# Performance work log

Hardware: AMD Instinct MI355X
Metric: run time of the kernel (lower is better)

The kernel has to match this reference:

```python
import jax, jax.numpy as jnp
import numpy as np

NODE_DIM = 8
IN_EDGE_DIM = 4
OUT_EDGE_DIM = 4
HID = 16
N_NODES = 100000
N_EDGES = 3200000
LN_EPS = 1e-5


def _layer_norm(h, gamma, beta):
    mu = jnp.mean(h, axis=-1, keepdims=True)
    var = jnp.mean(jnp.square(h - mu), axis=-1, keepdims=True)
    return (h - mu) * jax.lax.rsqrt(var + LN_EPS) * gamma + beta


def setup_inputs() -> dict:
    key = jax.random.key(0)
    ks = jax.random.split(key, 12)
    in_dim = NODE_DIM * 2 + IN_EDGE_DIM  # 20
    x = jax.random.normal(ks[0], (N_NODES, NODE_DIM), dtype=jnp.float32)
    edge_index = jax.random.randint(ks[1], (2, N_EDGES), 0, N_NODES, dtype=jnp.int64)
    edge_attr = jax.random.normal(ks[2], (N_EDGES, IN_EDGE_DIM), dtype=jnp.float32)
    # MLP params (Kaiming-uniform-ish scaling like torch defaults)
    def lin(k, fan_in, fan_out):
        lim = 1.0 / np.sqrt(fan_in)
        kw, kb = jax.random.split(k)
        W = jax.random.uniform(kw, (fan_in, fan_out), minval=-lim, maxval=lim, dtype=jnp.float32)
        b = jax.random.uniform(kb, (fan_out,), minval=-lim, maxval=lim, dtype=jnp.float32)
        return W, b
    W1, b1 = lin(ks[3], in_dim, HID)
    W2, b2 = lin(ks[4], HID, HID)
    W3, b3 = lin(ks[5], HID, OUT_EDGE_DIM)
    g1 = jnp.ones((HID,), jnp.float32); be1 = jnp.zeros((HID,), jnp.float32)
    g2 = jnp.ones((HID,), jnp.float32); be2 = jnp.zeros((HID,), jnp.float32)
    return {"x": x, "edge_index": edge_index, "edge_attr": edge_attr,
            "W1": W1, "b1": b1, "g1": g1, "be1": be1,
            "W2": W2, "b2": b2, "g2": g2, "be2": be2,
            "W3": W3, "b3": b3}


def reference(x, edge_index, edge_attr, W1, b1, g1, be1, W2, b2, g2, be2, W3, b3):
    frm = edge_index[0]
    to = edge_index[1]
    # gather node features for both endpoints, concat with edge features: [E, 2*node_dim+in_edge_dim]
    inpt = jnp.concatenate([x[frm], x[to], edge_attr.astype(jnp.float32)], axis=1)
    h = _layer_norm(jax.nn.relu(inpt @ W1 + b1), g1, be1)
    h = _layer_norm(jax.nn.relu(h @ W2 + b2), g2, be2)
    return h @ W3 + b3  # [E, out_edge_dim]
```

## Files before the change

### kernel.cpp

```cpp
#include <hip/hip_runtime.h>
#include <stdint.h>


using u16 = unsigned short;
using u32 = uint32_t;
typedef __attribute__((ext_vector_type(4))) float f32x4;
typedef __attribute__((ext_vector_type(8))) short bf16x8;
typedef __attribute__((ext_vector_type(2))) __bf16 bf16x2;

__device__ __forceinline__ float bf2f(u16 u) { return __uint_as_float(((u32)u) << 16); }
__device__ __forceinline__ float bflo(u32 u) { return __uint_as_float(u << 16); }
__device__ __forceinline__ float bfhi(u32 u) { return __uint_as_float(u & 0xFFFF0000u); }
__device__ __forceinline__ u32 f2bf(float f) {
    u32 u = __float_as_uint(f);
    return (u + 0x7FFFu + ((u >> 16) & 1u)) >> 16;
}
__device__ __forceinline__ u32 pkbf(float a, float b) {
    bf16x2 t;
    t.x = (__bf16)a;
    t.y = (__bf16)b;
    return __builtin_bit_cast(u32, t);
}
__device__ __forceinline__ float ldw(const void* p, int i, bool bf) {
    return bf ? bf2f(((const u16*)p)[i]) : ((const float*)p)[i];
}

#define WB_W1 0
#define WB_B1 320
#define WB_W2 336
#define WB_B2 592
#define WB_W3 608
#define WB_B3 672
#define WB_TOT 704
#define FQ_A1H 0
#define FQ_A1L 512
#define FQ_A2H 1024
#define FQ_A2L 1536
#define FQ_A3H 2048
#define FQ_A3L 2560
#define FB_OFF (WB_TOT + 1536)

__global__ __launch_bounds__(256)
void probe_convert(const int* __restrict__ ei, int n_pairs,
                   const void* W1, const void* b1, const void* g1, const void* be1,
                   const void* W2, const void* b2, const void* g2, const void* be2,
                   const void* W3, const void* b3,
                   int* __restrict__ flags, float* __restrict__ wb) {
    bool bf = (((const u32*)g1)[0] == 0x3F803F80u);
    __shared__ int s;
    if (threadIdx.x == 0) s = 0;
    __syncthreads();
    int limit = n_pairs < 2048 ? n_pairs : 2048;
    int found = 0;
    for (int i = threadIdx.x; i < limit; i += blockDim.x)
        if (ei[2 * i + 1] != 0) found = 1;
    if (found) s = 1;
    __syncthreads();
    if (threadIdx.x == 0) { flags[0] = s; flags[1] = bf ? 1 : 0; }

    int t = threadIdx.x;
    for (int i = t; i < 320; i += 256) wb[WB_W1 + i] = ldw(W1, i, bf);
    if (t < 16) wb[WB_B1 + t] = ldw(b1, t, bf);
    {
        int k = t >> 4;
        wb[WB_W2 + t] = ldw(g1, k, bf) * ldw(W2, t, bf);
    }
    if (t < 16) {
        float acc = ldw(b2, t, bf);
        for (int k = 0; k < 16; k++) acc = fmaf(ldw(be1, k, bf), ldw(W2, k * 16 + t, bf), acc);
        wb[WB_B2 + t] = acc;
    }
    if (t < 64) {
        int k = t >> 2;
        wb[WB_W3 + t] = ldw(g2, k, bf) * ldw(W3, t, bf);
    }
    if (t < 4) {
        float acc = ldw(b3, t, bf);
        for (int k = 0; k < 16; k++) acc = fmaf(ldw(be2, k, bf), ldw(W3, k * 4 + t, bf), acc);
        wb[WB_B3 + t] = acc;
    }
    if (t >= 4 && t < 32) wb[672 + t] = 0.f;

    __syncthreads();

    u16* fq = (u16*)(wb + WB_TOT);
    for (int i = t; i < 512; i += 256) {
        int l = i >> 3, j = i & 7;
        int m = l & 15, g = l >> 4;
        int k = g * 8 + j;
        int kk = k & 15;
        float w1 = (k < 20) ? wb[WB_W1 + k * 16 + m] : 0.f;
        u16 h1 = (u16)f2bf(w1);
        fq[FQ_A1H + i] = h1;
        fq[FQ_A1L + i] = (u16)f2bf(w1 - bf2f(h1));
        float w2 = wb[WB_W2 + kk * 16 + m];
        u16 h2 = (u16)f2bf(w2);
        fq[FQ_A2H + i] = h2;
        fq[FQ_A2L + i] = (u16)f2bf(w2 - bf2f(h2));
        float w3 = (m < 4) ? wb[WB_W3 + kk * 4 + m] : 0.f;
        u16 h3 = (u16)f2bf(w3);
        fq[FQ_A3H + i] = h3;
        fq[FQ_A3L + i] = (u16)f2bf(w3 - bf2f(h3));
    }
    {
        float* fbv = wb + FB_OFF;
        int l = t >> 2, r = t & 3;
        int row = ((l >> 4) << 2) + r;
        fbv[t] = wb[WB_B1 + row];
        fbv[256 + t] = wb[WB_B2 + row];
        fbv[512 + t] = (row < 4) ? wb[WB_B3 + row] : 0.f;
    }
}

__device__ __forceinline__ void ln16(f32x4 d, float& h0, float& h1, float& h2, float& h3) {
    f32x4 z = {0.f, 0.f, 0.f, 0.f};
    d = __builtin_elementwise_max(d, z);
    float s = (d.x + d.y) + (d.z + d.w);
    float q = fmaf(d.x, d.x, fmaf(d.y, d.y, fmaf(d.z, d.z, d.w * d.w)));
    s += __shfl_xor(s, 16);
    q += __shfl_xor(q, 16);
    s += __shfl_xor(s, 32);
    q += __shfl_xor(q, 32);
    float mu = s * 0.0625f;
    float var = fmaf(-mu, mu, q * 0.0625f);
    float r = rsqrtf(var + 1e-5f);
    float nb = -mu * r;
    h0 = fmaf(d.x, r, nb);
    h1 = fmaf(d.y, r, nb);
    h2 = fmaf(d.z, r, nb);
    h3 = fmaf(d.w, r, nb);
}

__device__ __forceinline__ bf16x8 redist_split(float h0, float h1, float h2, float h3,
                                               int n, int g) {
    u32 hi01 = pkbf(h0, h1), hi23 = pkbf(h2, h3);
    float r0 = h0 - bflo(hi01);
    float r1 = h1 - bfhi(hi01);
    float r2 = h2 - bflo(hi23);
    float r3 = h3 - bfhi(hi23);
    u32 lo01 = pkbf(r0, r1), lo23 = pkbf(r2, r3);
    int srcA = n + (((g & 1) << 1) << 4);
    int srcB = srcA + 16;
    u32 hA01 = (u32)__shfl((int)hi01, srcA);
    u32 hA23 = (u32)__shfl((int)hi23, srcA);
    u32 lA01 = (u32)__shfl((int)lo01, srcA);
    u32 lA23 = (u32)__shfl((int)lo23, srcA);
    u32 hB01 = (u32)__shfl((int)hi01, srcB);
    u32 hB23 = (u32)__shfl((int)hi23, srcB);
    u32 lB01 = (u32)__shfl((int)lo01, srcB);
    u32 lB23 = (u32)__shfl((int)lo23, srcB);
    bool hi = (g < 2);
    uint4 uu = make_uint4(hi ? hA01 : lA01, hi ? hA23 : lA23,
                          hi ? hB01 : lB01, hi ? hB23 : lB23);
    return __builtin_bit_cast(bf16x8, uu);
}

#define TPW 8

__global__ __launch_bounds__(256, 4)
void edge_mlp_mfma(const void* __restrict__ x, const int* __restrict__ ei,
                   const void* __restrict__ ea, const float* __restrict__ wb,
                   const int* __restrict__ flags, void* __restrict__ out, int n_edges) {
    const bool idx32 = flags[0] != 0;
    const bool bf = flags[1] != 0;

    const int lane = threadIdx.x & 63;
    const int n = lane & 15;
    const int g = lane >> 4;

    const u16* fq = (const u16*)(wb + WB_TOT);
    bf16x8 A1h = ((const bf16x8*)fq)[0 * 64 + lane];
    bf16x8 A1l = ((const bf16x8*)fq)[1 * 64 + lane];
    bf16x8 A2h = ((const bf16x8*)fq)[2 * 64 + lane];
    bf16x8 A2l = ((const bf16x8*)fq)[3 * 64 + lane];
    bf16x8 A3h = ((const bf16x8*)fq)[4 * 64 + lane];
    bf16x8 A3l = ((const bf16x8*)fq)[5 * 64 + lane];
    const f32x4* fb = (const f32x4*)(wb + FB_OFF);
    f32x4 pb1 = fb[lane];
    f32x4 pb2 = fb[64 + lane];
    f32x4 pb3 = fb[128 + lane];

    const int ntiles = (n_edges + 15) >> 4;
    const int wflat = blockIdx.x * 4 + (threadIdx.x >> 6);
    const int t0 = wflat * TPW;

#pragma unroll 1
    for (int ti = 0; ti < TPW; ++ti) {
        int tile = t0 + ti;
        if (tile >= ntiles) break;

        int e = (tile << 4) + n;
        bool ev = e < n_edges;

        int idx = 0;
        if (g < 2 && ev) {
            size_t col = (g == 0) ? (size_t)e : ((size_t)n_edges + (size_t)e);
            idx = idx32 ? ei[col] : ei[2 * col];
        }

        f32x4 d1 = pb1;
        if (bf) {
            uint4 raw = make_uint4(0u, 0u, 0u, 0u);
            if (g < 2) {
                raw = ((const uint4*)x)[idx];
            } else if (g == 2 && ev) {
                uint2 r = ((const uint2*)ea)[e];
                raw.x = r.x;
                raw.y = r.y;
            }
            d1 = __builtin_amdgcn_mfma_f32_16x16x32_bf16(
                A1h, __builtin_bit_cast(bf16x8, raw), d1, 0, 0, 0);
        } else {
            float f0 = 0.f, f1 = 0.f, f2 = 0.f, f3 = 0.f;
            float f4 = 0.f, f5 = 0.f, f6 = 0.f, f7 = 0.f;
            if (g < 2) {
                const float4* xp = (const float4*)x;
                float4 a = xp[2 * idx], b = xp[2 * idx + 1];
                f0 = a.x; f1 = a.y; f2 = a.z; f3 = a.w;
                f4 = b.x; f5 = b.y; f6 = b.z; f7 = b.w;
            } else if (g == 2 && ev) {
                float4 r = ((const float4*)ea)[e];
                f0 = r.x; f1 = r.y; f2 = r.z; f3 = r.w;
            }
            u32 h01 = pkbf(f0, f1), h23 = pkbf(f2, f3);
            u32 h45 = pkbf(f4, f5), h67 = pkbf(f6, f7);
            u32 l01 = pkbf(f0 - bflo(h01), f1 - bfhi(h01));
            u32 l23 = pkbf(f2 - bflo(h23), f3 - bfhi(h23));
            u32 l45 = pkbf(f4 - bflo(h45), f5 - bfhi(h45));
            u32 l67 = pkbf(f6 - bflo(h67), f7 - bfhi(h67));
            bf16x8 Bh = __builtin_bit_cast(bf16x8, make_uint4(h01, h23, h45, h67));
            bf16x8 Bl = __builtin_bit_cast(bf16x8, make_uint4(l01, l23, l45, l67));
            d1 = __builtin_amdgcn_mfma_f32_16x16x32_bf16(A1h, Bh, d1, 0, 0, 0);
            d1 = __builtin_amdgcn_mfma_f32_16x16x32_bf16(A1h, Bl, d1, 0, 0, 0);
            d1 = __builtin_amdgcn_mfma_f32_16x16x32_bf16(A1l, Bh, d1, 0, 0, 0);
        }

        float h0, h1, h2, h3;
        ln16(d1, h0, h1, h2, h3);

        bf16x8 f2v = redist_split(h0, h1, h2, h3, n, g);
        f32x4 d2 = pb2;
        d2 = __builtin_amdgcn_mfma_f32_16x16x32_bf16(A2h, f2v, d2, 0, 0, 0);
        d2 = __builtin_amdgcn_mfma_f32_16x16x32_bf16(A2l, f2v, d2, 0, 0, 0);
        float z0, z1, z2, z3;
        ln16(d2, z0, z1, z2, z3);

        bf16x8 f3v = redist_split(z0, z1, z2, z3, n, g);
        f32x4 d3 = pb3;
        d3 = __builtin_amdgcn_mfma_f32_16x16x32_bf16(A3h, f3v, d3, 0, 0, 0);
        d3 = __builtin_amdgcn_mfma_f32_16x16x32_bf16(A3l, f3v, d3, 0, 0, 0);

        if (g == 0 && ev) {
            if (bf) {
                u32 p0 = pkbf(d3.x, d3.y);
                u32 p1 = pkbf(d3.z, d3.w);
                ((uint2*)out)[e] = make_uint2(p0, p1);
            } else {
                ((float4*)out)[e] = make_float4(d3.x, d3.y, d3.z, d3.w);
            }
        }
    }
}

extern "C" void kernel_launch(void* const* d_in, const int* in_sizes, int n_in,
                              void* d_out, int out_size, void* d_ws, size_t ws_size,
                              hipStream_t stream) {
    const void* x  = d_in[0];
    const int* ei  = (const int*)d_in[1];
    const void* ea = d_in[2];

    int n_edges = in_sizes[1] / 2;

    int* flags = (int*)d_ws;
    float* wb = (float*)((char*)d_ws + 64);

    probe_convert<<<1, 256, 0, stream>>>(ei, n_edges,
                                         d_in[3], d_in[4], d_in[5], d_in[6],
                                         d_in[7], d_in[8], d_in[9], d_in[10],
                                         d_in[11], d_in[12], flags, wb);

    int ntiles = (n_edges + 15) / 16;
    int mblocks = (ntiles + 4 * TPW - 1) / (4 * TPW);
    edge_mlp_mfma<<<mblocks, 256, 0, stream>>>(x, ei, ea, wb, flags, d_out, n_edges);
}
```

Baseline: 214.4 us.

## Repack layer-2/3 weights to drop cross-lane shuffles and use branchless gathers

Reorders the layer-2 and layer-3 bf16 hi/lo weight fragments so each lane's own LayerNorm outputs (hi and lo parts) can feed the next MFMA directly as the B operand. This removes the eight ds_bpermute-style shuffles per layer that redistributed activations across lanes. The input gather becomes branchless: lanes that have no real data read from a zeroed scratch region in the weight buffer, and out-of-range edge indices are clamped. The tile loop is also unrolled by 2, which adds code size and register pressure and relies on the zero region staying zero.

```diff
diff --git a/kernel.cpp b/kernel.cpp
--- a/kernel.cpp
+++ b/kernel.cpp
@@ -32,12 +32,13 @@
 #define WB_W3 608
 #define WB_B3 672
 #define WB_TOT 704
+#define WB_ZRG 676
 #define FQ_A1H 0
 #define FQ_A1L 512
-#define FQ_A2H 1024
-#define FQ_A2L 1536
-#define FQ_A3H 2048
-#define FQ_A3L 2560
+#define FQ_A2X 1024
+#define FQ_A2Y 1536
+#define FQ_A3X 2048
+#define FQ_A3Y 2560
 #define FB_OFF (WB_TOT + 1536)
 
 __global__ __launch_bounds__(256)
@@ -87,20 +88,25 @@
     for (int i = t; i < 512; i += 256) {
         int l = i >> 3, j = i & 7;
         int m = l & 15, g = l >> 4;
-        int k = g * 8 + j;
-        int kk = k & 15;
-        float w1 = (k < 20) ? wb[WB_W1 + k * 16 + m] : 0.f;
+        int k1 = g * 8 + j;
+        float w1 = (k1 < 20) ? wb[WB_W1 + k1 * 16 + m] : 0.f;
         u16 h1 = (u16)f2bf(w1);
         fq[FQ_A1H + i] = h1;
         fq[FQ_A1L + i] = (u16)f2bf(w1 - bf2f(h1));
-        float w2 = wb[WB_W2 + kk * 16 + m];
+
+        int k2 = g * 4 + (j & 3);
+        int part = j >> 2;
+        float w2 = wb[WB_W2 + k2 * 16 + m];
         u16 h2 = (u16)f2bf(w2);
-        fq[FQ_A2H + i] = h2;
-        fq[FQ_A2L + i] = (u16)f2bf(w2 - bf2f(h2));
-        float w3 = (m < 4) ? wb[WB_W3 + kk * 4 + m] : 0.f;
+        u16 l2v = (u16)f2bf(w2 - bf2f(h2));
+        fq[FQ_A2X + i] = part ? l2v : h2;
+        fq[FQ_A2Y + i] = part ? h2 : l2v;
+
+        float w3 = (m < 4) ? wb[WB_W3 + k2 * 4 + m] : 0.f;
         u16 h3 = (u16)f2bf(w3);
-        fq[FQ_A3H + i] = h3;
-        fq[FQ_A3L + i] = (u16)f2bf(w3 - bf2f(h3));
+        u16 l3v = (u16)f2bf(w3 - bf2f(h3));
+        fq[FQ_A3X + i] = part ? l3v : h3;
+        fq[FQ_A3Y + i] = part ? h3 : l3v;
     }
     {
         float* fbv = wb + FB_OFF;
@@ -131,28 +137,11 @@
     h3 = fmaf(d.w, r, nb);
 }
 
-__device__ __forceinline__ bf16x8 redist_split(float h0, float h1, float h2, float h3,
-                                               int n, int g) {
+__device__ __forceinline__ bf16x8 packB(float h0, float h1, float h2, float h3) {
     u32 hi01 = pkbf(h0, h1), hi23 = pkbf(h2, h3);
-    float r0 = h0 - bflo(hi01);
-    float r1 = h1 - bfhi(hi01);
-    float r2 = h2 - bflo(hi23);
-    float r3 = h3 - bfhi(hi23);
-    u32 lo01 = pkbf(r0, r1), lo23 = pkbf(r2, r3);
-    int srcA = n + (((g & 1) << 1) << 4);
-    int srcB = srcA + 16;
-    u32 hA01 = (u32)__shfl((int)hi01, srcA);
-    u32 hA23 = (u32)__shfl((int)hi23, srcA);
-    u32 lA01 = (u32)__shfl((int)lo01, srcA);
-    u32 lA23 = (u32)__shfl((int)lo23, srcA);
-    u32 hB01 = (u32)__shfl((int)hi01, srcB);
-    u32 hB23 = (u32)__shfl((int)hi23, srcB);
-    u32 lB01 = (u32)__shfl((int)lo01, srcB);
-    u32 lB23 = (u32)__shfl((int)lo23, srcB);
-    bool hi = (g < 2);
-    uint4 uu = make_uint4(hi ? hA01 : lA01, hi ? hA23 : lA23,
-                          hi ? hB01 : lB01, hi ? hB23 : lB23);
-    return __builtin_bit_cast(bf16x8, uu);
+    u32 lo01 = pkbf(h0 - bflo(hi01), h1 - bfhi(hi01));
+    u32 lo23 = pkbf(h2 - bflo(hi23), h3 - bfhi(hi23));
+    return __builtin_bit_cast(bf16x8, make_uint4(hi01, hi23, lo01, lo23));
 }
 
 #define TPW 8
@@ -171,63 +160,64 @@
     const u16* fq = (const u16*)(wb + WB_TOT);
     bf16x8 A1h = ((const bf16x8*)fq)[0 * 64 + lane];
     bf16x8 A1l = ((const bf16x8*)fq)[1 * 64 + lane];
-    bf16x8 A2h = ((const bf16x8*)fq)[2 * 64 + lane];
-    bf16x8 A2l = ((const bf16x8*)fq)[3 * 64 + lane];
-    bf16x8 A3h = ((const bf16x8*)fq)[4 * 64 + lane];
-    bf16x8 A3l = ((const bf16x8*)fq)[5 * 64 + lane];
+    bf16x8 A2x = ((const bf16x8*)fq)[2 * 64 + lane];
+    bf16x8 A2y = ((const bf16x8*)fq)[3 * 64 + lane];
+    bf16x8 A3x = ((const bf16x8*)fq)[4 * 64 + lane];
+    bf16x8 A3y = ((const bf16x8*)fq)[5 * 64 + lane];
     const f32x4* fb = (const f32x4*)(wb + FB_OFF);
     f32x4 pb1 = fb[lane];
     f32x4 pb2 = fb[64 + lane];
     f32x4 pb3 = fb[128 + lane];
 
+    const char* zrg = (const char*)(wb + WB_ZRG);
+    const size_t eoff = (g == 1) ? (size_t)n_edges : 0;
+
     const int ntiles = (n_edges + 15) >> 4;
     const int wflat = blockIdx.x * 4 + (threadIdx.x >> 6);
     const int t0 = wflat * TPW;
 
-#pragma unroll 1
+#pragma unroll 2
     for (int ti = 0; ti < TPW; ++ti) {
         int tile = t0 + ti;
         if (tile >= ntiles) break;
 
         int e = (tile << 4) + n;
         bool ev = e < n_edges;
+        int ec = ev ? e : (n_edges - 1);
 
         int idx = 0;
-        if (g < 2 && ev) {
-            size_t col = (g == 0) ? (size_t)e : ((size_t)n_edges + (size_t)e);
+        if (g < 2) {
+            size_t col = eoff + (size_t)ec;
             idx = idx32 ? ei[col] : ei[2 * col];
         }
 
         f32x4 d1 = pb1;
         if (bf) {
-            uint4 raw = make_uint4(0u, 0u, 0u, 0u);
-            if (g < 2) {
-                raw = ((const uint4*)x)[idx];
-            } else if (g == 2 && ev) {
-                uint2 r = ((const uint2*)ea)[e];
-                raw.x = r.x;
-                raw.y = r.y;
-            }
+            const uint4* pA = (g < 2)
+                ? (const uint4*)((const char*)x + (size_t)idx * 16)
+                : (const uint4*)zrg;
+            const uint2* pE = (g == 2)
+                ? (const uint2*)((const char*)ea + (size_t)ec * 8)
+                : (const uint2*)zrg;
+            uint4 r16 = *pA;
+            uint2 r8 = *pE;
+            uint4 braw = make_uint4(r16.x | r8.x, r16.y | r8.y, r16.z, r16.w);
             d1 = __builtin_amdgcn_mfma_f32_16x16x32_bf16(
-                A1h, __builtin_bit_cast(bf16x8, raw), d1, 0, 0, 0);
+                A1h, __builtin_bit_cast(bf16x8, braw), d1, 0, 0, 0);
         } else {
-            float f0 = 0.f, f1 = 0.f, f2 = 0.f, f3 = 0.f;
-            float f4 = 0.f, f5 = 0.f, f6 = 0.f, f7 = 0.f;
-            if (g < 2) {
-                const float4* xp = (const float4*)x;
-                float4 a = xp[2 * idx], b = xp[2 * idx + 1];
-                f0 = a.x; f1 = a.y; f2 = a.z; f3 = a.w;
-                f4 = b.x; f5 = b.y; f6 = b.z; f7 = b.w;
-            } else if (g == 2 && ev) {
-                float4 r = ((const float4*)ea)[e];
-                f0 = r.x; f1 = r.y; f2 = r.z; f3 = r.w;
-            }
-            u32 h01 = pkbf(f0, f1), h23 = pkbf(f2, f3);
-            u32 h45 = pkbf(f4, f5), h67 = pkbf(f6, f7);
-            u32 l01 = pkbf(f0 - bflo(h01), f1 - bfhi(h01));
-            u32 l23 = pkbf(f2 - bflo(h23), f3 - bfhi(h23));
-            u32 l45 = pkbf(f4 - bflo(h45), f5 - bfhi(h45));
-            u32 l67 = pkbf(f6 - bflo(h67), f7 - bfhi(h67));
+            const float4* pA = (g < 2)
+                ? (const float4*)((const char*)x + (size_t)idx * 32)
+                : ((g == 2) ? (const float4*)((const char*)ea + (size_t)ec * 16)
+                            : (const float4*)zrg);
+            const float4* pB = (g < 2) ? (pA + 1) : (const float4*)zrg;
+            float4 a = *pA;
+            float4 b = *pB;
+            u32 h01 = pkbf(a.x, a.y), h23 = pkbf(a.z, a.w);
+            u32 h45 = pkbf(b.x, b.y), h67 = pkbf(b.z, b.w);
+            u32 l01 = pkbf(a.x - bflo(h01), a.y - bfhi(h01));
+            u32 l23 = pkbf(a.z - bflo(h23), a.w - bfhi(h23));
+            u32 l45 = pkbf(b.x - bflo(h45), b.y - bfhi(h45));
+            u32 l67 = pkbf(b.z - bflo(h67), b.w - bfhi(h67));
             bf16x8 Bh = __builtin_bit_cast(bf16x8, make_uint4(h01, h23, h45, h67));
             bf16x8 Bl = __builtin_bit_cast(bf16x8, make_uint4(l01, l23, l45, l67));
             d1 = __builtin_amdgcn_mfma_f32_16x16x32_bf16(A1h, Bh, d1, 0, 0, 0);
@@ -238,17 +228,17 @@
         float h0, h1, h2, h3;
         ln16(d1, h0, h1, h2, h3);
 
-        bf16x8 f2v = redist_split(h0, h1, h2, h3, n, g);
+        bf16x8 B2 = packB(h0, h1, h2, h3);
         f32x4 d2 = pb2;
-        d2 = __builtin_amdgcn_mfma_f32_16x16x32_bf16(A2h, f2v, d2, 0, 0, 0);
-        d2 = __builtin_amdgcn_mfma_f32_16x16x32_bf16(A2l, f2v, d2, 0, 0, 0);
+        d2 = __builtin_amdgcn_mfma_f32_16x16x32_bf16(A2x, B2, d2, 0, 0, 0);
+        d2 = __builtin_amdgcn_mfma_f32_16x16x32_bf16(A2y, B2, d2, 0, 0, 0);
         float z0, z1, z2, z3;
         ln16(d2, z0, z1, z2, z3);
 
-        bf16x8 f3v = redist_split(z0, z1, z2, z3, n, g);
+        bf16x8 B3 = packB(z0, z1, z2, z3);
         f32x4 d3 = pb3;
-        d3 = __builtin_amdgcn_mfma_f32_16x16x32_bf16(A3h, f3v, d3, 0, 0, 0);
-        d3 = __builtin_amdgcn_mfma_f32_16x16x32_bf16(A3l, f3v, d3, 0, 0, 0);
+        d3 = __builtin_amdgcn_mfma_f32_16x16x32_bf16(A3x, B3, d3, 0, 0, 0);
+        d3 = __builtin_amdgcn_mfma_f32_16x16x32_bf16(A3y, B3, d3, 0, 0, 0);
 
         if (g == 0 && ev) {
             if (bf) {
```

After: 227.1 us. +5.9%, slower.
